# Kernel optimization log

Measured on AMD Instinct MI355X. Metric: run time of the kernel, lower is better.

Reference implementation:

```python
import jax, jax.numpy as jnp
import numpy as np

L = 4          # n_layers
D_MODEL = 512
D_STATE = 32
D_INNER = 1024  # expand=2
D_CONV = 4
DT_RANK = 32    # ceil(d_model/16)
B = 8
T = 512


def setup_inputs() -> dict:
    key = jax.random.key(0)
    ks = jax.random.split(key, 12)
    s = 0.02
    x = jax.random.normal(ks[0], (B, T, D_MODEL), jnp.float32)
    in_w = jax.random.normal(ks[1], (L, D_MODEL, 2 * D_INNER), jnp.float32) * s
    conv_w = jax.random.normal(ks[2], (L, D_INNER, D_CONV), jnp.float32) * s
    conv_b = jnp.zeros((L, D_INNER), jnp.float32)
    xproj_w = jax.random.normal(ks[3], (L, D_INNER, DT_RANK + 2 * D_STATE), jnp.float32) * s
    dt_w = jax.random.normal(ks[4], (L, DT_RANK, D_INNER), jnp.float32) * s
    dt_b = jax.random.normal(ks[5], (L, D_INNER), jnp.float32) * 0.1
    # S4D-real init: A_log = log(1..d_state) per channel
    A_log = jnp.log(jnp.broadcast_to(jnp.arange(1, D_STATE + 1, dtype=jnp.float32), (L, D_INNER, D_STATE)))
    Dp = jnp.ones((L, D_INNER), jnp.float32)
    layer_out_w = jax.random.normal(ks[6], (L, D_INNER, D_MODEL), jnp.float32) * s
    ln_w = jnp.ones((L, D_MODEL), jnp.float32)
    ln_b = jnp.zeros((L, D_MODEL), jnp.float32)
    proj_w = jax.random.normal(ks[7], (D_MODEL, D_MODEL), jnp.float32) * s
    proj_b = jnp.zeros((D_MODEL,), jnp.float32)
    return dict(x=x, in_w=in_w, conv_w=conv_w, conv_b=conv_b, xproj_w=xproj_w,
                dt_w=dt_w, dt_b=dt_b, A_log=A_log, Dp=Dp, layer_out_w=layer_out_w,
                ln_w=ln_w, ln_b=ln_b, proj_w=proj_w, proj_b=proj_b)


def _layernorm(x, w, b, eps=1e-5):
    mu = jnp.mean(x, axis=-1, keepdims=True)
    var = jnp.mean(jnp.square(x - mu), axis=-1, keepdims=True)
    return (x - mu) * jax.lax.rsqrt(var + eps) * w + b


def _selective_scan(u, delta, A, Bm, Cm, D):
    # u, delta: (B,T,di); A: (di,ds); Bm, Cm: (B,T,ds); D: (di,)
    def step(h, inp):
        d_t, B_t, C_t, u_t = inp                      # (B,di),(B,ds),(B,ds),(B,di)
        dA = jnp.exp(d_t[..., None] * A)               # (B,di,ds)
        h = dA * h + (d_t * u_t)[..., None] * B_t[:, None, :]
        y = jnp.einsum('bdn,bn->bd', h, C_t)
        return h, y
    h0 = jnp.zeros((u.shape[0], A.shape[0], A.shape[1]), u.dtype)
    xs = (jnp.swapaxes(delta, 0, 1), jnp.swapaxes(Bm, 0, 1),
          jnp.swapaxes(Cm, 0, 1), jnp.swapaxes(u, 0, 1))
    _, ys = jax.lax.scan(step, h0, xs)                 # ys: (T,B,di)
    return jnp.swapaxes(ys, 0, 1) + u * D


def _mamba_layer(x, in_w, conv_w, conv_b, xproj_w, dt_w, dt_b, A_log, D, out_w):
    xz = x @ in_w                                      # (B,T,2*di)
    u, z = jnp.split(xz, 2, axis=-1)
    # causal depthwise conv1d over time
    uc = jnp.swapaxes(u, 1, 2)                         # (B,di,T)
    uc = jnp.pad(uc, ((0, 0), (0, 0), (D_CONV - 1, 0)))
    uc = jax.lax.conv_general_dilated(
        uc, conv_w[:, None, :], (1,), 'VALID',
        feature_group_count=D_INNER,
        dimension_numbers=('NCH', 'OIH', 'NCH')) + conv_b[None, :, None]
    u = jax.nn.silu(jnp.swapaxes(uc, 1, 2))            # (B,T,di)
    x_dbl = u @ xproj_w                                # (B,T,dt_rank+2*ds)
    dt, Bm, Cm = jnp.split(x_dbl, [DT_RANK, DT_RANK + D_STATE], axis=-1)
    delta = jax.nn.softplus(dt @ dt_w + dt_b)          # (B,T,di)
    A = -jnp.exp(A_log)                                # (di,ds)
    y = _selective_scan(u, delta, A, Bm, Cm, D)
    y = y * jax.nn.silu(z)
    return y @ out_w                                   # (B,T,d_model)


def reference(x, in_w, conv_w, conv_b, xproj_w, dt_w, dt_b, A_log, Dp,
              layer_out_w, ln_w, ln_b, proj_w, proj_b):
    for i in range(L):
        h = _layernorm(x, ln_w[i], ln_b[i])
        x = _mamba_layer(h, in_w[i], conv_w[i], conv_b[i], xproj_w[i],
                         dt_w[i], dt_b[i], A_log[i], Dp[i], layer_out_w[i]) + x
    return x @ proj_w + proj_b
```

## Files before the change

kernel.cpp:

```cpp
#include <hip/hip_runtime.h>
#include <math.h>

#define LNUM 4
#define DM 512
#define DS 32
#define DI 1024
#define DTR 32
#define NB 8
#define NT 512
#define MROWS (NB*NT)
#define NCH (NB*DI)
#define NCHUNK 16
#define TCH (NT/NCHUNK)
#define SSTATES (NCH*DS)

typedef __attribute__((ext_vector_type(8))) short short8;
typedef __attribute__((ext_vector_type(4))) float floatx4;
typedef unsigned short ushort_t;

__device__ __forceinline__ float sigmoidf_(float x){ return 1.f/(1.f+__expf(-x)); }
__device__ __forceinline__ float exp2f_(float x){ return __builtin_amdgcn_exp2f(x); }

__device__ __forceinline__ unsigned short rne_bf16(float f){
  unsigned int u = __float_as_uint(f);
  u += 0x7fffu + ((u >> 16) & 1u);
  return (unsigned short)(u >> 16);
}

__device__ __forceinline__ void load_lds16(const void* g, void* l){
  __builtin_amdgcn_global_load_lds(
      (const __attribute__((address_space(1))) void*)g,
      (__attribute__((address_space(3))) void*)l, 16, 0, 0);
}

__global__ __launch_bounds__(256) void ln_k(const float* __restrict__ x,
    const float* __restrict__ w, const float* __restrict__ b, ushort_t* __restrict__ out)
{
  int row = blockIdx.x;
  const float* xr = x + (size_t)row*DM;
  float v0 = xr[threadIdx.x];
  float v1 = xr[threadIdx.x + 256];
  float s = v0+v1, sq = v0*v0+v1*v1;
  #pragma unroll
  for (int off=32; off>0; off>>=1) { s += __shfl_xor(s, off, 64); sq += __shfl_xor(sq, off, 64); }
  __shared__ float ls[4], lq[4];
  int wid = threadIdx.x >> 6;
  if ((threadIdx.x & 63)==0){ ls[wid]=s; lq[wid]=sq; }
  __syncthreads();
  s  = ls[0]+ls[1]+ls[2]+ls[3];
  sq = lq[0]+lq[1]+lq[2]+lq[3];
  float mean = s * (1.f/DM);
  float var  = sq * (1.f/DM) - mean*mean;
  float rstd = rsqrtf(var + 1e-5f);
  int c0 = threadIdx.x, c1 = threadIdx.x+256;
  out[(size_t)row*DM + c0] = rne_bf16((v0-mean)*rstd*w[c0] + b[c0]);
  out[(size_t)row*DM + c1] = rne_bf16((v1-mean)*rstd*w[c1] + b[c1]);
}

__global__ __launch_bounds__(256) void wprep_k(const float* __restrict__ src,
    ushort_t* __restrict__ dst, int K, int N)
{
  src += (size_t)blockIdx.z * K * N;
  dst += (size_t)blockIdx.z * N * K;
  int n0 = blockIdx.x * 64, k0 = blockIdx.y * 64;
  __shared__ float t[64][65];
  int tid = threadIdx.x;
  int cr = tid >> 6, cc = tid & 63;
  #pragma unroll
  for (int i=0;i<16;i++){
    int k = k0 + i*4 + cr, n = n0 + cc;
    float v = (k < K && n < N) ? src[(size_t)k*N + n] : 0.f;
    t[i*4+cr][cc] = v;
  }
  __syncthreads();
  #pragma unroll
  for (int i=0;i<16;i++){
    int n = n0 + i*4 + cr, k = k0 + cc;
    if (n < N && k < K) dst[(size_t)n*K + k] = rne_bf16(t[cc][i*4+cr]);
  }
}

enum { AE_SPLIT=0, AE_STORE=1, AE_RESIDBF=2, AE_BIAS=3 };

template<int BN, int FN, int EPI>
__global__ __launch_bounds__(256) void agemm_k(
    const ushort_t* __restrict__ A, int K,
    const ushort_t* __restrict__ Wt,
    float* __restrict__ C0, float* __restrict__ C1,
    ushort_t* __restrict__ Cb, int ldc,
    const float* __restrict__ bias)
{
  constexpr int WN = BN/2;
  constexpr int LW4 = BN/32;
  __shared__ __align__(16) ushort_t As[128*64];
  __shared__ __align__(16) ushort_t Ws[BN*64];
  int tid = threadIdx.x;
  int w = tid >> 6, lane = tid & 63;
  int wr = w >> 1, wc = w & 1;
  int quad = lane >> 4, l16 = lane & 15;
  int mBase = blockIdx.y * 128;
  int nBase = blockIdx.x * BN;

  int lr = lane >> 3, ls = lane & 7;
  int sg = ls ^ lr;

  const ushort_t* gA[4]; ushort_t* lA[4];
  #pragma unroll
  for (int j=0;j<4;j++){
    int r0 = (w*4+j)*8;
    gA[j] = A + (size_t)(mBase + r0 + lr)*K + sg*8;
    lA[j] = &As[r0*64];
  }
  const ushort_t* gW[LW4]; ushort_t* lW[LW4];
  #pragma unroll
  for (int c=0;c<LW4;c++){
    int r0 = (w*LW4+c)*8;
    gW[c] = Wt + (size_t)(nBase + r0 + lr)*K + sg*8;
    lW[c] = &Ws[r0*64];
  }

  floatx4 acc[4][FN];
  #pragma unroll
  for (int i=0;i<4;i++)
    #pragma unroll
    for (int j=0;j<FN;j++) acc[i][j] = (floatx4){0.f,0.f,0.f,0.f};

  for (int it=0; it<K; it+=64){
    #pragma unroll
    for (int j=0;j<4;j++) load_lds16(gA[j], lA[j]);
    #pragma unroll
    for (int c=0;c<LW4;c++) load_lds16(gW[c], lW[c]);
    __syncthreads();
    #pragma unroll
    for (int ks=0;ks<2;ks++){
      short8 aF[4], bF[FN];
      #pragma unroll
      for (int i=0;i<4;i++)
        aF[i] = *(const short8*)&As[(wr*64+i*16+l16)*64 + ((((ks<<2)|quad))^(l16&7))*8];
      #pragma unroll
      for (int j=0;j<FN;j++)
        bF[j] = *(const short8*)&Ws[(wc*WN+j*16+l16)*64 + ((((ks<<2)|quad))^(l16&7))*8];
      #pragma unroll
      for (int i=0;i<4;i++)
        #pragma unroll
        for (int j=0;j<FN;j++)
          acc[i][j] = __builtin_amdgcn_mfma_f32_16x16x32_bf16(aF[i], bF[j], acc[i][j], 0, 0, 0);
    }
    __syncthreads();
    #pragma unroll
    for (int j=0;j<4;j++) gA[j] += 64;
    #pragma unroll
    for (int c=0;c<LW4;c++) gW[c] += 64;
  }

  #pragma unroll
  for (int i=0;i<4;i++){
    #pragma unroll
    for (int j=0;j<FN;j++){
      int n = nBase + wc*WN + j*16 + l16;
      #pragma unroll
      for (int r=0;r<4;r++){
        int m = mBase + wr*64 + i*16 + quad*4 + r;
        float v = acc[i][j][r];
        if (EPI == AE_SPLIT)       { if (n < DI) C0[(size_t)m*DI + n] = v;
                                     else        C1[(size_t)m*DI + (n-DI)] = v; }
        else if (EPI == AE_STORE)  { C0[(size_t)m*ldc + n] = v; }
        else if (EPI == AE_RESIDBF){ float nv = C0[(size_t)m*ldc + n] + v;
                                     C0[(size_t)m*ldc + n] = nv;
                                     Cb[(size_t)m*ldc + n] = rne_bf16(nv); }
        else                       { C0[(size_t)m*ldc + n] = v + bias[n]; }
      }
    }
  }
}

__global__ __launch_bounds__(256) void gemm32_k(
    const float* __restrict__ A, int lda, int K,
    const ushort_t* __restrict__ Wt,
    float* __restrict__ C0, int ldc, const float* __restrict__ bias)
{
  constexpr int STR = 40;
  __shared__ __align__(16) short As[128*STR];
  __shared__ __align__(16) short Ws[128*STR];
  int tid = threadIdx.x;
  int w = tid >> 6, lane = tid & 63;
  int wr = w >> 1, wc = w & 1;
  int quad = lane >> 4, l16 = lane & 15;
  int mBase = blockIdx.y * 128;
  int nBase = blockIdx.x * 128;

  floatx4 acc[4][4];
  #pragma unroll
  for (int i=0;i<4;i++)
    #pragma unroll
    for (int j=0;j<4;j++) acc[i][j] = (floatx4){0.f,0.f,0.f,0.f};

  int sRow = tid >> 3, kv = tid & 7;
  for (int k0 = 0; k0 < K; k0 += 32) {
    #pragma unroll
    for (int i=0;i<4;i++){
      int r = sRow + i*32;
      floatx4 v = *(const floatx4*)&A[(size_t)(mBase+r)*lda + k0 + kv*4];
      unsigned int p0 = (unsigned int)rne_bf16(v.x) | ((unsigned int)rne_bf16(v.y) << 16);
      unsigned int p1 = (unsigned int)rne_bf16(v.z) | ((unsigned int)rne_bf16(v.w) << 16);
      uint2 pk; pk.x = p0; pk.y = p1;
      *(uint2*)&As[r*STR + kv*4] = pk;
    }
    #pragma unroll
    for (int i=0;i<4;i++){
      int r = sRow + i*32;
      uint2 wv = *(const uint2*)&Wt[(size_t)(nBase+r)*K + k0 + kv*4];
      *(uint2*)&Ws[r*STR + kv*4] = wv;
    }
    __syncthreads();
    short8 aF[4], bF[4];
    #pragma unroll
    for (int i=0;i<4;i++)
      aF[i] = *(const short8*)&As[(wr*64 + i*16 + l16)*STR + quad*8];
    #pragma unroll
    for (int j=0;j<4;j++)
      bF[j] = *(const short8*)&Ws[(wc*64 + j*16 + l16)*STR + quad*8];
    #pragma unroll
    for (int i=0;i<4;i++)
      #pragma unroll
      for (int j=0;j<4;j++)
        acc[i][j] = __builtin_amdgcn_mfma_f32_16x16x32_bf16(aF[i], bF[j], acc[i][j], 0, 0, 0);
    __syncthreads();
  }
  #pragma unroll
  for (int i=0;i<4;i++){
    #pragma unroll
    for (int j=0;j<4;j++){
      int n = nBase + wc*64 + j*16 + l16;
      #pragma unroll
      for (int r=0;r<4;r++){
        int m = mBase + wr*64 + i*16 + quad*4 + r;
        float t = acc[i][j][r] + bias[n];
        C0[(size_t)m*ldc + n] = (t > 20.f) ? t : log1pf(__expf(t));
      }
    }
  }
}

__global__ __launch_bounds__(256) void conv_k(const float* __restrict__ u,
    const float* __restrict__ cw, const float* __restrict__ cb,
    float* __restrict__ uc, ushort_t* __restrict__ ucbf)
{
  int g = blockIdx.x*256 + threadIdx.x;
  int d = g & (DI-1);
  int m = g >> 10;
  int t = m & (NT-1);
  float w0=cw[d*4+0], w1=cw[d*4+1], w2=cw[d*4+2], w3=cw[d*4+3];
  float acc = cb[d];
  acc += w3 * u[(size_t)m*DI + d];
  if (t>=1) acc += w2*u[(size_t)(m-1)*DI+d];
  if (t>=2) acc += w1*u[(size_t)(m-2)*DI+d];
  if (t>=3) acc += w0*u[(size_t)(m-3)*DI+d];
  float s = acc * sigmoidf_(acc);
  uc[(size_t)m*DI+d] = s;
  ucbf[(size_t)m*DI+d] = rne_bf16(s);
}

__global__ __launch_bounds__(256,2) void scan_carry_k(
    const float* __restrict__ delta, const float* __restrict__ uc,
    const float* __restrict__ xdbl, const float* __restrict__ A_log,
    float* __restrict__ Ebuf, float* __restrict__ Hbuf)
{
  int ch = blockIdx.x*256 + threadIdx.x;
  int b = ch >> 10, d = ch & (DI-1);
  int chunk = blockIdx.y;
  int r0 = b*NT + chunk*TCH;
  float Ac[DS], h[DS], E[DS];
  const floatx4* Arow = (const floatx4*)(A_log + (size_t)d*DS);
  #pragma unroll
  for (int j=0;j<8;j++){
    floatx4 a = Arow[j];
    Ac[4*j+0] = -__expf(a.x)*1.44269504f;
    Ac[4*j+1] = -__expf(a.y)*1.44269504f;
    Ac[4*j+2] = -__expf(a.z)*1.44269504f;
    Ac[4*j+3] = -__expf(a.w)*1.44269504f;
  }
  #pragma unroll
  for (int n=0;n<DS;n++){ h[n]=0.f; E[n]=1.f; }
  const float* dp = delta + (size_t)r0*DI + d;
  const float* up = uc    + (size_t)r0*DI + d;
  const float* xb = xdbl  + (size_t)r0*96 + 32;
  float dv = dp[0], uv = up[0];
  for (int t=0;t<TCH;t++){
    int tn = (t+1<TCH)?(t+1):t;
    float dvn = dp[(size_t)tn*DI];
    float uvn = up[(size_t)tn*DI];
    const floatx4* Br = (const floatx4*)(xb + (size_t)t*96);
    float du = dv*uv;
    #pragma unroll
    for (int j=0;j<8;j++){
      floatx4 Bv = Br[j];
      float e0 = exp2f_(dv*Ac[4*j+0]); h[4*j+0]=fmaf(e0,h[4*j+0],du*Bv.x); E[4*j+0]*=e0;
      float e1 = exp2f_(dv*Ac[4*j+1]); h[4*j+1]=fmaf(e1,h[4*j+1],du*Bv.y); E[4*j+1]*=e1;
      float e2 = exp2f_(dv*Ac[4*j+2]); h[4*j+2]=fmaf(e2,h[4*j+2],du*Bv.z); E[4*j+2]*=e2;
      float e3 = exp2f_(dv*Ac[4*j+3]); h[4*j+3]=fmaf(e3,h[4*j+3],du*Bv.w); E[4*j+3]*=e3;
    }
    dv=dvn; uv=uvn;
  }
  size_t o = ((size_t)chunk*NCH + ch)*DS;
  #pragma unroll
  for (int j=0;j<8;j++){
    *(floatx4*)&Ebuf[o + 4*j] = (floatx4){E[4*j],E[4*j+1],E[4*j+2],E[4*j+3]};
    *(floatx4*)&Hbuf[o + 4*j] = (floatx4){h[4*j],h[4*j+1],h[4*j+2],h[4*j+3]};
  }
}

__global__ __launch_bounds__(256) void scan_combine_k(float* __restrict__ base)
{
  int s = blockIdx.x*256 + threadIdx.x;
  float h = 0.f;
  base[s] = 0.f;
  #pragma unroll
  for (int c=1;c<NCHUNK;c++){
    size_t p = (size_t)(c-1)*SSTATES + s;
    float E = base[SSTATES + p];
    float H = base[(size_t)NCHUNK*SSTATES + p];
    h = fmaf(E, h, H);
    base[(size_t)c*SSTATES + s] = h;
  }
}

__global__ __launch_bounds__(256,2) void scan_apply_k(
    const float* __restrict__ delta, const float* __restrict__ uc,
    const float* __restrict__ zbuf, const float* __restrict__ xdbl,
    const float* __restrict__ A_log, const float* __restrict__ Dp,
    const float* __restrict__ Hin, ushort_t* __restrict__ y)
{
  int ch = blockIdx.x*256 + threadIdx.x;
  int b = ch >> 10, d = ch & (DI-1);
  int chunk = blockIdx.y;
  int r0 = b*NT + chunk*TCH;
  float Ac[DS], h[DS];
  const floatx4* Arow = (const floatx4*)(A_log + (size_t)d*DS);
  #pragma unroll
  for (int j=0;j<8;j++){
    floatx4 a = Arow[j];
    Ac[4*j+0] = -__expf(a.x)*1.44269504f;
    Ac[4*j+1] = -__expf(a.y)*1.44269504f;
    Ac[4*j+2] = -__expf(a.z)*1.44269504f;
    Ac[4*j+3] = -__expf(a.w)*1.44269504f;
  }
  size_t o = (size_t)chunk*SSTATES + (size_t)ch*DS;
  #pragma unroll
  for (int j=0;j<8;j++){
    floatx4 hv = *(const floatx4*)&Hin[o + 4*j];
    h[4*j]=hv.x; h[4*j+1]=hv.y; h[4*j+2]=hv.z; h[4*j+3]=hv.w;
  }
  float Dv = Dp[d];
  const float* dp = delta + (size_t)r0*DI + d;
  const float* up = uc    + (size_t)r0*DI + d;
  const float* zp = zbuf  + (size_t)r0*DI + d;
  const float* xb = xdbl  + (size_t)r0*96;
  float dv = dp[0], uv = up[0], zv = zp[0];
  for (int t=0;t<TCH;t++){
    int tn = (t+1<TCH)?(t+1):t;
    float dvn = dp[(size_t)tn*DI];
    float uvn = up[(size_t)tn*DI];
    float zvn = zp[(size_t)tn*DI];
    const floatx4* Br = (const floatx4*)(xb + (size_t)t*96 + 32);
    const floatx4* Cr = (const floatx4*)(xb + (size_t)t*96 + 64);
    float du = dv*uv;
    float acc = 0.f;
    #pragma unroll
    for (int j=0;j<8;j++){
      floatx4 Bv = Br[j];
      floatx4 Cv = Cr[j];
      float e0 = exp2f_(dv*Ac[4*j+0]); h[4*j+0]=fmaf(e0,h[4*j+0],du*Bv.x); acc=fmaf(h[4*j+0],Cv.x,acc);
      float e1 = exp2f_(dv*Ac[4*j+1]); h[4*j+1]=fmaf(e1,h[4*j+1],du*Bv.y); acc=fmaf(h[4*j+1],Cv.y,acc);
      float e2 = exp2f_(dv*Ac[4*j+2]); h[4*j+2]=fmaf(e2,h[4*j+2],du*Bv.z); acc=fmaf(h[4*j+2],Cv.z,acc);
      float e3 = exp2f_(dv*Ac[4*j+3]); h[4*j+3]=fmaf(e3,h[4*j+3],du*Bv.w); acc=fmaf(h[4*j+3],Cv.w,acc);
    }
    float yv = acc + uv*Dv;
    y[(size_t)(r0+t)*DI + d] = rne_bf16(yv * (zv * sigmoidf_(zv)));
    dv=dvn; uv=uvn; zv=zvn;
  }
}

extern "C" void kernel_launch(void* const* d_in, const int* in_sizes, int n_in,
                              void* d_out, int out_size, void* d_ws, size_t ws_size,
                              hipStream_t stream) {
  const float* x       = (const float*)d_in[0];
  const float* in_w    = (const float*)d_in[1];
  const float* conv_w  = (const float*)d_in[2];
  const float* conv_b  = (const float*)d_in[3];
  const float* xproj_w = (const float*)d_in[4];
  const float* dt_w    = (const float*)d_in[5];
  const float* dt_b    = (const float*)d_in[6];
  const float* A_log   = (const float*)d_in[7];
  const float* Dp      = (const float*)d_in[8];
  const float* low     = (const float*)d_in[9];
  const float* ln_w    = (const float*)d_in[10];
  const float* ln_b    = (const float*)d_in[11];
  const float* proj_w  = (const float*)d_in[12];
  const float* proj_b  = (const float*)d_in[13];
  float* out = (float*)d_out;

  float* ws   = (float*)d_ws;
  float* xcur = ws;
  float* u0   = xcur + (size_t)MROWS*DM;
  float* zb   = u0   + (size_t)MROWS*DI;
  float* ucb  = zb   + (size_t)MROWS*DI;
  float* xdbl = ucb  + (size_t)MROWS*DI;
  float* dl   = xdbl + (size_t)MROWS*96;
  ushort_t* hn_bf   = (ushort_t*)(dl + (size_t)MROWS*DI);
  ushort_t* ucb_bf  = hn_bf  + (size_t)MROWS*DM;
  ushort_t* xcur_bf = ucb_bf + (size_t)MROWS*DI;
  ushort_t* inw_t   = xcur_bf + (size_t)MROWS*DM;
  ushort_t* xprj_t  = inw_t  + (size_t)LNUM*2*DI*DM;
  ushort_t* dtw_t   = xprj_t + (size_t)LNUM*96*DI;
  ushort_t* low_t   = dtw_t  + (size_t)LNUM*DI*DTR;
  ushort_t* prj_t   = low_t  + (size_t)LNUM*DM*DI;
  float* scb = (float*)(prj_t + (size_t)DM*DM);
  ushort_t* y_bf = (ushort_t*)u0;

  hipMemcpyAsync(xcur, x, sizeof(float)*(size_t)MROWS*DM, hipMemcpyDeviceToDevice, stream);

  wprep_k<<<dim3(32, 8, LNUM), 256, 0, stream>>>(in_w,    inw_t,  DM, 2*DI);
  wprep_k<<<dim3(2, 16, LNUM), 256, 0, stream>>>(xproj_w, xprj_t, DI, 96);
  wprep_k<<<dim3(16, 1, LNUM), 256, 0, stream>>>(dt_w,    dtw_t,  DTR, DI);
  wprep_k<<<dim3(8, 16, LNUM), 256, 0, stream>>>(low,     low_t,  DI, DM);
  wprep_k<<<dim3(8, 8, 1),     256, 0, stream>>>(proj_w,  prj_t,  DM, DM);

  for (int l=0; l<LNUM; l++){
    ln_k<<<MROWS, 256, 0, stream>>>(xcur, ln_w + l*DM, ln_b + l*DM, hn_bf);
    agemm_k<128,4,AE_SPLIT><<<dim3(16,32), 256, 0, stream>>>(
        hn_bf, DM, inw_t + (size_t)l*2*DI*DM, u0, zb, nullptr, 0, nullptr);
    conv_k<<<(MROWS*DI)/256, 256, 0, stream>>>(u0, conv_w + l*DI*4, conv_b + l*DI, ucb, ucb_bf);
    agemm_k<96,3,AE_STORE><<<dim3(1,32), 256, 0, stream>>>(
        ucb_bf, DI, xprj_t + (size_t)l*96*DI, xdbl, nullptr, nullptr, 96, nullptr);
    gemm32_k<<<dim3(8,32), 256, 0, stream>>>(
        xdbl, 96, DTR, dtw_t + (size_t)l*DI*DTR, dl, DI, dt_b + l*DI);
    scan_carry_k<<<dim3(NCH/256, NCHUNK-1), 256, 0, stream>>>(
        dl, ucb, xdbl, A_log + (size_t)l*DI*DS, scb + SSTATES, scb + (size_t)NCHUNK*SSTATES);
    scan_combine_k<<<SSTATES/256, 256, 0, stream>>>(scb);
    scan_apply_k<<<dim3(NCH/256, NCHUNK), 256, 0, stream>>>(
        dl, ucb, zb, xdbl, A_log + (size_t)l*DI*DS, Dp + l*DI, scb, y_bf);
    agemm_k<128,4,AE_RESIDBF><<<dim3(4,32), 256, 0, stream>>>(
        y_bf, DI, low_t + (size_t)l*DM*DI, xcur, nullptr, xcur_bf, DM, nullptr);
  }
  agemm_k<128,4,AE_BIAS><<<dim3(4,32), 256, 0, stream>>>(
      xcur_bf, DM, prj_t, out, nullptr, nullptr, DM, proj_b);
}
```

Baseline: 968.3 us.

## Rework chunked selective scan, store z/u in bf16, split-K x_proj GEMM

The chunked scan now uses 32 chunks and stores only the chunk's summed delta instead of per-state decay products. The combine step recomputes the decay as exp2(A*S) and is parallelised four ways per channel. B/C rows are staged in shared memory, z and the conv output are kept only in bf16 (dropping the fp32 copies), and the x_proj GEMM uses split-K with atomicAdd into a buffer zeroed beforehand, raising occupancy of the scan kernels. This trades extra launches, nondeterministic atomic accumulation and slightly lower precision of u and z inputs for less memory traffic and more parallelism.

```diff
diff --git a/kernel.cpp b/kernel.cpp
--- a/kernel.cpp
+++ b/kernel.cpp
@@ -10,7 +10,7 @@
 #define NT 512
 #define MROWS (NB*NT)
 #define NCH (NB*DI)
-#define NCHUNK 16
+#define NCHUNK 32
 #define TCH (NT/NCHUNK)
 #define SSTATES (NCH*DS)
 
@@ -20,6 +20,7 @@
 
 __device__ __forceinline__ float sigmoidf_(float x){ return 1.f/(1.f+__expf(-x)); }
 __device__ __forceinline__ float exp2f_(float x){ return __builtin_amdgcn_exp2f(x); }
+__device__ __forceinline__ float bf2f(ushort_t u){ return __uint_as_float(((unsigned)u)<<16); }
 
 __device__ __forceinline__ unsigned short rne_bf16(float f){
   unsigned int u = __float_as_uint(f);
@@ -80,13 +81,17 @@
   }
 }
 
+__global__ __launch_bounds__(256) void zero_k(float* __restrict__ p){
+  ((floatx4*)p)[blockIdx.x*256 + threadIdx.x] = (floatx4){0.f,0.f,0.f,0.f};
+}
+
 enum { AE_SPLIT=0, AE_STORE=1, AE_RESIDBF=2, AE_BIAS=3 };
 
 template<int BN, int FN, int EPI>
 __global__ __launch_bounds__(256) void agemm_k(
     const ushort_t* __restrict__ A, int K,
     const ushort_t* __restrict__ Wt,
-    float* __restrict__ C0, float* __restrict__ C1,
+    float* __restrict__ C0, ushort_t* __restrict__ Zb,
     ushort_t* __restrict__ Cb, int ldc,
     const float* __restrict__ bias)
 {
@@ -163,12 +168,91 @@
         int m = mBase + wr*64 + i*16 + quad*4 + r;
         float v = acc[i][j][r];
         if (EPI == AE_SPLIT)       { if (n < DI) C0[(size_t)m*DI + n] = v;
-                                     else        C1[(size_t)m*DI + (n-DI)] = v; }
+                                     else        Zb[(size_t)m*DI + (n-DI)] = rne_bf16(v); }
         else if (EPI == AE_STORE)  { C0[(size_t)m*ldc + n] = v; }
         else if (EPI == AE_RESIDBF){ float nv = C0[(size_t)m*ldc + n] + v;
                                      C0[(size_t)m*ldc + n] = nv;
                                      Cb[(size_t)m*ldc + n] = rne_bf16(nv); }
         else                       { C0[(size_t)m*ldc + n] = v + bias[n]; }
+      }
+    }
+  }
+}
+
+__global__ __launch_bounds__(256) void agemm_splitk_k(
+    const ushort_t* __restrict__ A, int K, int kseg,
+    const ushort_t* __restrict__ Wt, float* __restrict__ C0, int ldc)
+{
+  constexpr int BN = 96, FN = 3, WN = 48, LW4 = 3;
+  __shared__ __align__(16) ushort_t As[128*64];
+  __shared__ __align__(16) ushort_t Ws[BN*64];
+  int tid = threadIdx.x;
+  int w = tid >> 6, lane = tid & 63;
+  int wr = w >> 1, wc = w & 1;
+  int quad = lane >> 4, l16 = lane & 15;
+  int mBase = blockIdx.y * 128;
+  int nBase = 0;
+  int kOff = blockIdx.z * kseg;
+
+  int lr = lane >> 3, ls = lane & 7;
+  int sg = ls ^ lr;
+
+  const ushort_t* gA[4]; ushort_t* lA[4];
+  #pragma unroll
+  for (int j=0;j<4;j++){
+    int r0 = (w*4+j)*8;
+    gA[j] = A + (size_t)(mBase + r0 + lr)*K + kOff + sg*8;
+    lA[j] = &As[r0*64];
+  }
+  const ushort_t* gW[LW4]; ushort_t* lW[LW4];
+  #pragma unroll
+  for (int c=0;c<LW4;c++){
+    int r0 = (w*LW4+c)*8;
+    gW[c] = Wt + (size_t)(nBase + r0 + lr)*K + kOff + sg*8;
+    lW[c] = &Ws[r0*64];
+  }
+  floatx4 acc[4][FN];
+  #pragma unroll
+  for (int i=0;i<4;i++)
+    #pragma unroll
+    for (int j=0;j<FN;j++) acc[i][j] = (floatx4){0.f,0.f,0.f,0.f};
+
+  for (int it=0; it<kseg; it+=64){
+    #pragma unroll
+    for (int j=0;j<4;j++) load_lds16(gA[j], lA[j]);
+    #pragma unroll
+    for (int c=0;c<LW4;c++) load_lds16(gW[c], lW[c]);
+    __syncthreads();
+    #pragma unroll
+    for (int ks=0;ks<2;ks++){
+      short8 aF[4], bF[FN];
+      #pragma unroll
+      for (int i=0;i<4;i++)
+        aF[i] = *(const short8*)&As[(wr*64+i*16+l16)*64 + ((((ks<<2)|quad))^(l16&7))*8];
+      #pragma unroll
+      for (int j=0;j<FN;j++)
+        bF[j] = *(const short8*)&Ws[(wc*WN+j*16+l16)*64 + ((((ks<<2)|quad))^(l16&7))*8];
+      #pragma unroll
+      for (int i=0;i<4;i++)
+        #pragma unroll
+        for (int j=0;j<FN;j++)
+          acc[i][j] = __builtin_amdgcn_mfma_f32_16x16x32_bf16(aF[i], bF[j], acc[i][j], 0, 0, 0);
+    }
+    __syncthreads();
+    #pragma unroll
+    for (int j=0;j<4;j++) gA[j] += 64;
+    #pragma unroll
+    for (int c=0;c<LW4;c++) gW[c] += 64;
+  }
+  #pragma unroll
+  for (int i=0;i<4;i++){
+    #pragma unroll
+    for (int j=0;j<FN;j++){
+      int n = wc*WN + j*16 + l16;
+      #pragma unroll
+      for (int r=0;r<4;r++){
+        int m = mBase + wr*64 + i*16 + quad*4 + r;
+        atomicAdd(&C0[(size_t)m*ldc + n], acc[i][j][r]);
       }
     }
   }
@@ -244,7 +328,7 @@
 
 __global__ __launch_bounds__(256) void conv_k(const float* __restrict__ u,
     const float* __restrict__ cw, const float* __restrict__ cb,
-    float* __restrict__ uc, ushort_t* __restrict__ ucbf)
+    ushort_t* __restrict__ ucbf)
 {
   int g = blockIdx.x*256 + threadIdx.x;
   int d = g & (DI-1);
@@ -257,20 +341,25 @@
   if (t>=2) acc += w1*u[(size_t)(m-2)*DI+d];
   if (t>=3) acc += w0*u[(size_t)(m-3)*DI+d];
   float s = acc * sigmoidf_(acc);
-  uc[(size_t)m*DI+d] = s;
   ucbf[(size_t)m*DI+d] = rne_bf16(s);
 }
 
-__global__ __launch_bounds__(256,2) void scan_carry_k(
-    const float* __restrict__ delta, const float* __restrict__ uc,
+__global__ __launch_bounds__(256,4) void scan_carry_k(
+    const float* __restrict__ delta, const ushort_t* __restrict__ ucbf,
     const float* __restrict__ xdbl, const float* __restrict__ A_log,
-    float* __restrict__ Ebuf, float* __restrict__ Hbuf)
-{
-  int ch = blockIdx.x*256 + threadIdx.x;
+    float* __restrict__ Sbuf, float* __restrict__ Hloc)
+{
+  __shared__ __align__(16) float Bs[TCH][32];
+  int tid = threadIdx.x;
+  int ch = blockIdx.x*256 + tid;
   int b = ch >> 10, d = ch & (DI-1);
   int chunk = blockIdx.y;
   int r0 = b*NT + chunk*TCH;
-  float Ac[DS], h[DS], E[DS];
+  {
+    int t = tid >> 4, p = tid & 15;
+    *(float2*)&Bs[t][p*2] = *(const float2*)(xdbl + (size_t)(r0+t)*96 + 32 + p*2);
+  }
+  float Ac[DS];
   const floatx4* Arow = (const floatx4*)(A_log + (size_t)d*DS);
   #pragma unroll
   for (int j=0;j<8;j++){
@@ -280,62 +369,90 @@
     Ac[4*j+2] = -__expf(a.z)*1.44269504f;
     Ac[4*j+3] = -__expf(a.w)*1.44269504f;
   }
-  #pragma unroll
-  for (int n=0;n<DS;n++){ h[n]=0.f; E[n]=1.f; }
+  float h[DS];
+  #pragma unroll
+  for (int n=0;n<DS;n++) h[n]=0.f;
+  float S = 0.f;
   const float* dp = delta + (size_t)r0*DI + d;
-  const float* up = uc    + (size_t)r0*DI + d;
-  const float* xb = xdbl  + (size_t)r0*96 + 32;
-  float dv = dp[0], uv = up[0];
+  const ushort_t* up = ucbf + (size_t)r0*DI + d;
+  __syncthreads();
+  float dv = dp[0], uv = bf2f(up[0]);
   for (int t=0;t<TCH;t++){
     int tn = (t+1<TCH)?(t+1):t;
     float dvn = dp[(size_t)tn*DI];
-    float uvn = up[(size_t)tn*DI];
-    const floatx4* Br = (const floatx4*)(xb + (size_t)t*96);
+    float uvn = bf2f(up[(size_t)tn*DI]);
     float du = dv*uv;
+    S += dv;
     #pragma unroll
     for (int j=0;j<8;j++){
-      floatx4 Bv = Br[j];
-      float e0 = exp2f_(dv*Ac[4*j+0]); h[4*j+0]=fmaf(e0,h[4*j+0],du*Bv.x); E[4*j+0]*=e0;
-      float e1 = exp2f_(dv*Ac[4*j+1]); h[4*j+1]=fmaf(e1,h[4*j+1],du*Bv.y); E[4*j+1]*=e1;
-      float e2 = exp2f_(dv*Ac[4*j+2]); h[4*j+2]=fmaf(e2,h[4*j+2],du*Bv.z); E[4*j+2]*=e2;
-      float e3 = exp2f_(dv*Ac[4*j+3]); h[4*j+3]=fmaf(e3,h[4*j+3],du*Bv.w); E[4*j+3]*=e3;
+      floatx4 Bv = *(const floatx4*)&Bs[t][4*j];
+      float e0 = exp2f_(dv*Ac[4*j+0]); h[4*j+0]=fmaf(e0,h[4*j+0],du*Bv.x);
+      float e1 = exp2f_(dv*Ac[4*j+1]); h[4*j+1]=fmaf(e1,h[4*j+1],du*Bv.y);
+      float e2 = exp2f_(dv*Ac[4*j+2]); h[4*j+2]=fmaf(e2,h[4*j+2],du*Bv.z);
+      float e3 = exp2f_(dv*Ac[4*j+3]); h[4*j+3]=fmaf(e3,h[4*j+3],du*Bv.w);
     }
     dv=dvn; uv=uvn;
   }
+  Sbuf[(size_t)chunk*NCH + ch] = S;
   size_t o = ((size_t)chunk*NCH + ch)*DS;
   #pragma unroll
-  for (int j=0;j<8;j++){
-    *(floatx4*)&Ebuf[o + 4*j] = (floatx4){E[4*j],E[4*j+1],E[4*j+2],E[4*j+3]};
-    *(floatx4*)&Hbuf[o + 4*j] = (floatx4){h[4*j],h[4*j+1],h[4*j+2],h[4*j+3]};
-  }
-}
-
-__global__ __launch_bounds__(256) void scan_combine_k(float* __restrict__ base)
-{
-  int s = blockIdx.x*256 + threadIdx.x;
-  float h = 0.f;
-  base[s] = 0.f;
-  #pragma unroll
+  for (int j=0;j<8;j++)
+    *(floatx4*)&Hloc[o + 4*j] = (floatx4){h[4*j],h[4*j+1],h[4*j+2],h[4*j+3]};
+}
+
+__global__ __launch_bounds__(256) void scan_combine_k(
+    const float* __restrict__ Sbuf, const float* __restrict__ Hloc,
+    const float* __restrict__ A_log, float* __restrict__ Hin)
+{
+  int g = blockIdx.x*256 + threadIdx.x;
+  int ch = g >> 2, q = g & 3;
+  int d = ch & (DI-1);
+  float Ac[8];
+  #pragma unroll
+  for (int j=0;j<2;j++){
+    floatx4 a = *(const floatx4*)(A_log + (size_t)d*DS + q*8 + 4*j);
+    Ac[4*j+0] = -__expf(a.x)*1.44269504f;
+    Ac[4*j+1] = -__expf(a.y)*1.44269504f;
+    Ac[4*j+2] = -__expf(a.z)*1.44269504f;
+    Ac[4*j+3] = -__expf(a.w)*1.44269504f;
+  }
+  float h[8];
+  #pragma unroll
+  for (int n=0;n<8;n++) h[n]=0.f;
+  size_t so = (size_t)ch*DS + q*8;
+  *(floatx4*)&Hin[so]   = (floatx4){0.f,0.f,0.f,0.f};
+  *(floatx4*)&Hin[so+4] = (floatx4){0.f,0.f,0.f,0.f};
   for (int c=1;c<NCHUNK;c++){
-    size_t p = (size_t)(c-1)*SSTATES + s;
-    float E = base[SSTATES + p];
-    float H = base[(size_t)NCHUNK*SSTATES + p];
-    h = fmaf(E, h, H);
-    base[(size_t)c*SSTATES + s] = h;
-  }
-}
-
-__global__ __launch_bounds__(256,2) void scan_apply_k(
-    const float* __restrict__ delta, const float* __restrict__ uc,
-    const float* __restrict__ zbuf, const float* __restrict__ xdbl,
+    float S = Sbuf[(size_t)(c-1)*NCH + ch];
+    size_t p = (size_t)(c-1)*SSTATES + so;
+    floatx4 H0 = *(const floatx4*)&Hloc[p];
+    floatx4 H1 = *(const floatx4*)&Hloc[p+4];
+    float Hl[8] = {H0.x,H0.y,H0.z,H0.w,H1.x,H1.y,H1.z,H1.w};
+    #pragma unroll
+    for (int n=0;n<8;n++) h[n] = fmaf(exp2f_(Ac[n]*S), h[n], Hl[n]);
+    size_t oo = (size_t)c*SSTATES + so;
+    *(floatx4*)&Hin[oo]   = (floatx4){h[0],h[1],h[2],h[3]};
+    *(floatx4*)&Hin[oo+4] = (floatx4){h[4],h[5],h[6],h[7]};
+  }
+}
+
+__global__ __launch_bounds__(256,4) void scan_apply_k(
+    const float* __restrict__ delta, const ushort_t* __restrict__ ucbf,
+    const ushort_t* __restrict__ zbf, const float* __restrict__ xdbl,
     const float* __restrict__ A_log, const float* __restrict__ Dp,
     const float* __restrict__ Hin, ushort_t* __restrict__ y)
 {
-  int ch = blockIdx.x*256 + threadIdx.x;
+  __shared__ __align__(16) float BCs[TCH][64];
+  int tid = threadIdx.x;
+  int ch = blockIdx.x*256 + tid;
   int b = ch >> 10, d = ch & (DI-1);
   int chunk = blockIdx.y;
   int r0 = b*NT + chunk*TCH;
-  float Ac[DS], h[DS];
+  {
+    int t = tid >> 4, p = tid & 15;
+    *(floatx4*)&BCs[t][p*4] = *(const floatx4*)(xdbl + (size_t)(r0+t)*96 + 32 + p*4);
+  }
+  float Ac[DS];
   const floatx4* Arow = (const floatx4*)(A_log + (size_t)d*DS);
   #pragma unroll
   for (int j=0;j<8;j++){
@@ -345,6 +462,7 @@
     Ac[4*j+2] = -__expf(a.z)*1.44269504f;
     Ac[4*j+3] = -__expf(a.w)*1.44269504f;
   }
+  float h[DS];
   size_t o = (size_t)chunk*SSTATES + (size_t)ch*DS;
   #pragma unroll
   for (int j=0;j<8;j++){
@@ -353,23 +471,21 @@
   }
   float Dv = Dp[d];
   const float* dp = delta + (size_t)r0*DI + d;
-  const float* up = uc    + (size_t)r0*DI + d;
-  const float* zp = zbuf  + (size_t)r0*DI + d;
-  const float* xb = xdbl  + (size_t)r0*96;
-  float dv = dp[0], uv = up[0], zv = zp[0];
+  const ushort_t* up = ucbf + (size_t)r0*DI + d;
+  const ushort_t* zp = zbf  + (size_t)r0*DI + d;
+  __syncthreads();
+  float dv = dp[0], uv = bf2f(up[0]), zv = bf2f(zp[0]);
   for (int t=0;t<TCH;t++){
     int tn = (t+1<TCH)?(t+1):t;
     float dvn = dp[(size_t)tn*DI];
-    float uvn = up[(size_t)tn*DI];
-    float zvn = zp[(size_t)tn*DI];
-    const floatx4* Br = (const floatx4*)(xb + (size_t)t*96 + 32);
-    const floatx4* Cr = (const floatx4*)(xb + (size_t)t*96 + 64);
+    float uvn = bf2f(up[(size_t)tn*DI]);
+    float zvn = bf2f(zp[(size_t)tn*DI]);
     float du = dv*uv;
     float acc = 0.f;
     #pragma unroll
     for (int j=0;j<8;j++){
-      floatx4 Bv = Br[j];
-      floatx4 Cv = Cr[j];
+      floatx4 Bv = *(const floatx4*)&BCs[t][4*j];
+      floatx4 Cv = *(const floatx4*)&BCs[t][32+4*j];
       float e0 = exp2f_(dv*Ac[4*j+0]); h[4*j+0]=fmaf(e0,h[4*j+0],du*Bv.x); acc=fmaf(h[4*j+0],Cv.x,acc);
       float e1 = exp2f_(dv*Ac[4*j+1]); h[4*j+1]=fmaf(e1,h[4*j+1],du*Bv.y); acc=fmaf(h[4*j+1],Cv.y,acc);
       float e2 = exp2f_(dv*Ac[4*j+2]); h[4*j+2]=fmaf(e2,h[4*j+2],du*Bv.z); acc=fmaf(h[4*j+2],Cv.z,acc);
@@ -403,19 +519,20 @@
   float* ws   = (float*)d_ws;
   float* xcur = ws;
   float* u0   = xcur + (size_t)MROWS*DM;
-  float* zb   = u0   + (size_t)MROWS*DI;
-  float* ucb  = zb   + (size_t)MROWS*DI;
-  float* xdbl = ucb  + (size_t)MROWS*DI;
+  float* xdbl = u0   + (size_t)MROWS*DI;
   float* dl   = xdbl + (size_t)MROWS*96;
   ushort_t* hn_bf   = (ushort_t*)(dl + (size_t)MROWS*DI);
-  ushort_t* ucb_bf  = hn_bf  + (size_t)MROWS*DM;
-  ushort_t* xcur_bf = ucb_bf + (size_t)MROWS*DI;
+  ushort_t* zb_bf   = hn_bf   + (size_t)MROWS*DM;
+  ushort_t* ucb_bf  = zb_bf   + (size_t)MROWS*DI;
+  ushort_t* xcur_bf = ucb_bf  + (size_t)MROWS*DI;
   ushort_t* inw_t   = xcur_bf + (size_t)MROWS*DM;
   ushort_t* xprj_t  = inw_t  + (size_t)LNUM*2*DI*DM;
   ushort_t* dtw_t   = xprj_t + (size_t)LNUM*96*DI;
   ushort_t* low_t   = dtw_t  + (size_t)LNUM*DI*DTR;
   ushort_t* prj_t   = low_t  + (size_t)LNUM*DM*DI;
-  float* scb = (float*)(prj_t + (size_t)DM*DM);
+  float* Sbuf = (float*)(prj_t + (size_t)DM*DM);
+  float* Hloc = Sbuf + (size_t)(NCHUNK-1)*NCH;
+  float* Hin  = Hloc + (size_t)(NCHUNK-1)*SSTATES;
   ushort_t* y_bf = (ushort_t*)u0;
 
   hipMemcpyAsync(xcur, x, sizeof(float)*(size_t)MROWS*DM, hipMemcpyDeviceToDevice, stream);
@@ -429,17 +546,19 @@
   for (int l=0; l<LNUM; l++){
     ln_k<<<MROWS, 256, 0, stream>>>(xcur, ln_w + l*DM, ln_b + l*DM, hn_bf);
     agemm_k<128,4,AE_SPLIT><<<dim3(16,32), 256, 0, stream>>>(
-        hn_bf, DM, inw_t + (size_t)l*2*DI*DM, u0, zb, nullptr, 0, nullptr);
-    conv_k<<<(MROWS*DI)/256, 256, 0, stream>>>(u0, conv_w + l*DI*4, conv_b + l*DI, ucb, ucb_bf);
-    agemm_k<96,3,AE_STORE><<<dim3(1,32), 256, 0, stream>>>(
-        ucb_bf, DI, xprj_t + (size_t)l*96*DI, xdbl, nullptr, nullptr, 96, nullptr);
+        hn_bf, DM, inw_t + (size_t)l*2*DI*DM, u0, zb_bf, nullptr, 0, nullptr);
+    conv_k<<<(MROWS*DI)/256, 256, 0, stream>>>(u0, conv_w + l*DI*4, conv_b + l*DI, ucb_bf);
+    zero_k<<<(MROWS*96/4)/256, 256, 0, stream>>>(xdbl);
+    agemm_splitk_k<<<dim3(1,32,4), 256, 0, stream>>>(
+        ucb_bf, DI, DI/4, xprj_t + (size_t)l*96*DI, xdbl, 96);
     gemm32_k<<<dim3(8,32), 256, 0, stream>>>(
         xdbl, 96, DTR, dtw_t + (size_t)l*DI*DTR, dl, DI, dt_b + l*DI);
     scan_carry_k<<<dim3(NCH/256, NCHUNK-1), 256, 0, stream>>>(
-        dl, ucb, xdbl, A_log + (size_t)l*DI*DS, scb + SSTATES, scb + (size_t)NCHUNK*SSTATES);
-    scan_combine_k<<<SSTATES/256, 256, 0, stream>>>(scb);
+        dl, ucb_bf, xdbl, A_log + (size_t)l*DI*DS, Sbuf, Hloc);
+    scan_combine_k<<<(NCH*4)/256, 256, 0, stream>>>(
+        Sbuf, Hloc, A_log + (size_t)l*DI*DS, Hin);
     scan_apply_k<<<dim3(NCH/256, NCHUNK), 256, 0, stream>>>(
-        dl, ucb, zb, xdbl, A_log + (size_t)l*DI*DS, Dp + l*DI, scb, y_bf);
+        dl, ucb_bf, zb_bf, xdbl, A_log + (size_t)l*DI*DS, Dp + l*DI, Hin, y_bf);
     agemm_k<128,4,AE_RESIDBF><<<dim3(4,32), 256, 0, stream>>>(
         y_bf, DI, low_t + (size_t)l*DM*DI, xcur, nullptr, xcur_bf, DM, nullptr);
   }
```

New measurement: 918.9 us. -5.1%, faster.
